# Performance work log

Measured on AMD Instinct MI355X. Metric: run time of the kernel, lower is better.

The kernel has to match this reference:

```python
import jax, jax.numpy as jnp
import numpy as np

N_NODES = 10000
N_EDGES = 640000
D = 128


def setup_inputs() -> dict:
    key = jax.random.key(0)
    k1, k2, k3, k4 = jax.random.split(key, 4)
    X = jax.random.normal(k1, (N_NODES, D), dtype=jnp.float32)
    Y = jax.random.normal(k2, (N_EDGES, D), dtype=jnp.float32)
    # nn.Linear(in, out, bias=False): weight shape (out, in), y = Y @ W.T
    W = jax.random.normal(k3, (D, D), dtype=jnp.float32) * (1.0 / np.sqrt(D))
    edge_index = jax.random.randint(k4, (N_EDGES, 2), 0, N_NODES, dtype=jnp.int64)
    return {"X": X, "Y": Y, "W": W, "edge_index": edge_index}


def reference(X, Y, W, edge_index):
    # Edge transform: (E, d_in) @ (d_in, d_out) -> (E, d_out)
    Y_prime = jnp.einsum('ei,oi->eo', Y, W)
    # Scatter-add transformed edge features to source nodes
    src = edge_index[:, 0]
    agg = jax.ops.segment_sum(Y_prime, src, num_segments=X.shape[0])  # (N, d_out)
    # Residual + activation
    X_prime = jax.nn.relu(X + agg)
    return (X_prime, Y_prime)
```

## Files before the change

### kernel.cpp

```cpp
#include <hip/hip_runtime.h>

#define N_NODES 10000
#define N_EDGES 640000
#define DD 128

typedef __attribute__((ext_vector_type(8))) short short8;
typedef __attribute__((ext_vector_type(8))) float f32x8;
typedef __attribute__((ext_vector_type(4))) float f32x4;
typedef __attribute__((ext_vector_type(2))) float f32x2;

__device__ __forceinline__ unsigned pack_bf2(float lo, float hi) {
  return __builtin_amdgcn_perm(__float_as_uint(hi), __float_as_uint(lo), 0x07060302u);
}

__device__ __forceinline__ void stage_w(const float* __restrict__ W,
                                        short8* lwr) {
  const int tid = threadIdx.x;
#pragma unroll
  for (int t = 0; t < 8; ++t) {
    int s = t * 256 + tid;
    f32x8 v = *(const f32x8*)(W + (size_t)s * 8);
    short8 av;
    unsigned* au = (unsigned*)&av;
    au[0] = pack_bf2(v[0], v[1]);
    au[1] = pack_bf2(v[2], v[3]);
    au[2] = pack_bf2(v[4], v[5]);
    au[3] = pack_bf2(v[6], v[7]);
    int j = s >> 4;
    int c = s & 15;
    lwr[(j << 4) | (c ^ (j & 7))] = av;
  }
  __syncthreads();
}

__global__ __launch_bounds__(256) void k_hist(const int* __restrict__ EI,
                                              int* __restrict__ count) {
  const int e = blockIdx.x * 256 + threadIdx.x;
  atomicAdd(&count[EI[2 * e]], 1);
}

__global__ __launch_bounds__(1024) void k_scan(const int* __restrict__ count,
                                               int* __restrict__ rowptr,
                                               int* __restrict__ cursor) {
  __shared__ int part[1024];
  const int tid = threadIdx.x;
  const int base = tid * 10;
  int local[10];
  int s = 0;
#pragma unroll
  for (int i = 0; i < 10; ++i) {
    const int idx = base + i;
    const int v = (idx < N_NODES) ? count[idx] : 0;
    local[i] = s;
    s += v;
  }
  part[tid] = s;
  __syncthreads();
  for (int off = 1; off < 1024; off <<= 1) {
    int v = 0;
    if (tid >= off) v = part[tid - off];
    __syncthreads();
    if (tid >= off) part[tid] += v;
    __syncthreads();
  }
  const int excl = (tid > 0) ? part[tid - 1] : 0;
#pragma unroll
  for (int i = 0; i < 10; ++i) {
    const int idx = base + i;
    if (idx < N_NODES) {
      const int r = excl + local[i];
      rowptr[idx] = r;
      cursor[idx] = r;
    }
  }
  if (tid == 1023) rowptr[N_NODES] = part[1023];
}

__global__ __launch_bounds__(256) void k_fill(const int* __restrict__ EI,
                                              int* __restrict__ cursor,
                                              int* __restrict__ col) {
  const int e = blockIdx.x * 256 + threadIdx.x;
  const int s = EI[2 * e];
  const int pos = atomicAdd(&cursor[s], 1);
  col[pos] = e;
}

__global__ __launch_bounds__(256, 2) void k_gemm_big(
    const float* __restrict__ Y,
    const float* __restrict__ W,
    float* __restrict__ Yp) {
  __shared__ short8 lwr[2048];
  stage_w(W, lwr);
  const int wid  = threadIdx.x >> 6;
  const int lane = threadIdx.x & 63;
  const int l15  = lane & 15;
  const int lg   = lane >> 4;
  const int koff = lg * 8;

#pragma unroll 1
  for (int ch = 0; ch < 2; ++ch) {
    const int ebase = (blockIdx.x * 2 + ch) * 128 + wid * 32;

    short8 a[2][4];
#pragma unroll
    for (int mt = 0; mt < 2; ++mt) {
      const float* yr = Y + (size_t)(ebase + mt * 16 + l15) * DD;
#pragma unroll
      for (int kk = 0; kk < 4; ++kk) {
        f32x8 v = *(const f32x8*)(yr + kk * 32 + koff);
        short8 av;
        unsigned* au = (unsigned*)&av;
        au[0] = pack_bf2(v[0], v[1]);
        au[1] = pack_bf2(v[2], v[3]);
        au[2] = pack_bf2(v[4], v[5]);
        au[3] = pack_bf2(v[6], v[7]);
        a[mt][kk] = av;
      }
    }

    f32x4 acc[2][8];
#pragma unroll
    for (int mt = 0; mt < 2; ++mt)
#pragma unroll
      for (int nt = 0; nt < 8; ++nt)
        acc[mt][nt] = (f32x4){0.f, 0.f, 0.f, 0.f};

#pragma unroll
    for (int nt = 0; nt < 8; ++nt) {
      const int j = nt * 16 + l15;
#pragma unroll
      for (int kk = 0; kk < 4; ++kk) {
        const int kc = kk * 4 + lg;
        short8 b = lwr[(j << 4) | (kc ^ (j & 7))];
        acc[0][nt] = __builtin_amdgcn_mfma_f32_16x16x32_bf16(a[0][kk], b, acc[0][nt], 0, 0, 0);
        acc[1][nt] = __builtin_amdgcn_mfma_f32_16x16x32_bf16(a[1][kk], b, acc[1][nt], 0, 0, 0);
      }
    }

    const int r0 = lg * 4;
#pragma unroll
    for (int mt = 0; mt < 2; ++mt) {
#pragma unroll
      for (int reg = 0; reg < 4; ++reg) {
        float* orow = Yp + (size_t)(ebase + mt * 16 + r0 + reg) * DD + l15;
#pragma unroll
        for (int nt = 0; nt < 8; ++nt)
          orow[nt * 16] = acc[mt][nt][reg];
      }
    }
  }
}

__global__ __launch_bounds__(256) void k_gather(
    const float* __restrict__ Yp,
    const int* __restrict__ rowptr,
    const int* __restrict__ col,
    const float* __restrict__ X,
    float* __restrict__ Xp) {
  const int node = blockIdx.x * 4 + (threadIdx.x >> 6);
  const int lane = threadIdx.x & 63;
  const size_t co = 2 * lane;
  const int b  = rowptr[node];
  const int en = rowptr[node + 1];

  f32x2 acc = *(const f32x2*)(X + (size_t)node * DD + co);
  int i = b;
  for (; i + 4 <= en; i += 4) {
    const int e0 = col[i], e1 = col[i + 1], e2 = col[i + 2], e3 = col[i + 3];
    f32x2 v0 = *(const f32x2*)(Yp + (size_t)e0 * DD + co);
    f32x2 v1 = *(const f32x2*)(Yp + (size_t)e1 * DD + co);
    f32x2 v2 = *(const f32x2*)(Yp + (size_t)e2 * DD + co);
    f32x2 v3 = *(const f32x2*)(Yp + (size_t)e3 * DD + co);
    acc += v0; acc += v1; acc += v2; acc += v3;
  }
  for (; i < en; ++i) {
    const int e0 = col[i];
    acc += *(const f32x2*)(Yp + (size_t)e0 * DD + co);
  }
  f32x2 r;
  r[0] = acc[0] > 0.f ? acc[0] : 0.f;
  r[1] = acc[1] > 0.f ? acc[1] : 0.f;
  *(f32x2*)(Xp + (size_t)node * DD + co) = r;
}

extern "C" void kernel_launch(void* const* d_in, const int* in_sizes, int n_in,
                              void* d_out, int out_size, void* d_ws, size_t ws_size,
                              hipStream_t stream) {
  const float* X  = (const float*)d_in[0];
  const float* Y  = (const float*)d_in[1];
  const float* W  = (const float*)d_in[2];
  const int*   EI = (const int*)d_in[3];

  float* Xp = (float*)d_out;
  float* Yp = Xp + (size_t)N_NODES * DD;

  int* w      = (int*)d_ws;
  int* count  = w;
  int* rowptr = w + 10000;
  int* cursor = w + 20001;
  int* col    = w + 30001;

  hipMemsetAsync(count, 0, N_NODES * sizeof(int), stream);
  k_hist<<<N_EDGES / 256, 256, 0, stream>>>(EI, count);
  k_scan<<<1, 1024, 0, stream>>>(count, rowptr, cursor);
  k_fill<<<N_EDGES / 256, 256, 0, stream>>>(EI, cursor, col);
  k_gemm_big<<<2500, 256, 0, stream>>>(Y, W, Yp);
  k_gather<<<2500, 256, 0, stream>>>(Yp, rowptr, col, X, Xp);
}
```

Baseline: 316.0 us.

## Use nontemporal Y loads, raise GEMM occupancy, unroll gather by 8, kernel memset

Several small tweaks at once. Y is read with nontemporal loads so it streams past the caches, and the GEMM launch bound moves from 2 to 4 blocks per CU. The gather loop unrolls to 8 edges to keep more loads in flight, and hipMemsetAsync is replaced by a small zeroing kernel. The tighter launch bound may force register spills in the GEMM, since each wave holds 16 accumulator vectors plus 8 A fragments.

```diff
diff --git a/kernel.cpp b/kernel.cpp
--- a/kernel.cpp
+++ b/kernel.cpp
@@ -33,6 +33,11 @@
   __syncthreads();
 }
 
+__global__ __launch_bounds__(256) void k_zero(int* __restrict__ count) {
+  const int i = blockIdx.x * 256 + threadIdx.x;
+  if (i < N_NODES) count[i] = 0;
+}
+
 __global__ __launch_bounds__(256) void k_hist(const int* __restrict__ EI,
                                               int* __restrict__ count) {
   const int e = blockIdx.x * 256 + threadIdx.x;
@@ -85,7 +90,7 @@
   col[pos] = e;
 }
 
-__global__ __launch_bounds__(256, 2) void k_gemm_big(
+__global__ __launch_bounds__(256, 4) void k_gemm_big(
     const float* __restrict__ Y,
     const float* __restrict__ W,
     float* __restrict__ Yp) {
@@ -107,13 +112,15 @@
       const float* yr = Y + (size_t)(ebase + mt * 16 + l15) * DD;
 #pragma unroll
       for (int kk = 0; kk < 4; ++kk) {
-        f32x8 v = *(const f32x8*)(yr + kk * 32 + koff);
+        const f32x4* p = (const f32x4*)(yr + kk * 32 + koff);
+        f32x4 v0 = __builtin_nontemporal_load(p);
+        f32x4 v1 = __builtin_nontemporal_load(p + 1);
         short8 av;
         unsigned* au = (unsigned*)&av;
-        au[0] = pack_bf2(v[0], v[1]);
-        au[1] = pack_bf2(v[2], v[3]);
-        au[2] = pack_bf2(v[4], v[5]);
-        au[3] = pack_bf2(v[6], v[7]);
+        au[0] = pack_bf2(v0[0], v0[1]);
+        au[1] = pack_bf2(v0[2], v0[3]);
+        au[2] = pack_bf2(v1[0], v1[1]);
+        au[3] = pack_bf2(v1[2], v1[3]);
         a[mt][kk] = av;
       }
     }
@@ -165,17 +172,20 @@
 
   f32x2 acc = *(const f32x2*)(X + (size_t)node * DD + co);
   int i = b;
-  for (; i + 4 <= en; i += 4) {
-    const int e0 = col[i], e1 = col[i + 1], e2 = col[i + 2], e3 = col[i + 3];
-    f32x2 v0 = *(const f32x2*)(Yp + (size_t)e0 * DD + co);
-    f32x2 v1 = *(const f32x2*)(Yp + (size_t)e1 * DD + co);
-    f32x2 v2 = *(const f32x2*)(Yp + (size_t)e2 * DD + co);
-    f32x2 v3 = *(const f32x2*)(Yp + (size_t)e3 * DD + co);
+  for (; i + 8 <= en; i += 8) {
+    f32x2 v0 = *(const f32x2*)(Yp + (size_t)col[i]     * DD + co);
+    f32x2 v1 = *(const f32x2*)(Yp + (size_t)col[i + 1] * DD + co);
+    f32x2 v2 = *(const f32x2*)(Yp + (size_t)col[i + 2] * DD + co);
+    f32x2 v3 = *(const f32x2*)(Yp + (size_t)col[i + 3] * DD + co);
+    f32x2 v4 = *(const f32x2*)(Yp + (size_t)col[i + 4] * DD + co);
+    f32x2 v5 = *(const f32x2*)(Yp + (size_t)col[i + 5] * DD + co);
+    f32x2 v6 = *(const f32x2*)(Yp + (size_t)col[i + 6] * DD + co);
+    f32x2 v7 = *(const f32x2*)(Yp + (size_t)col[i + 7] * DD + co);
     acc += v0; acc += v1; acc += v2; acc += v3;
+    acc += v4; acc += v5; acc += v6; acc += v7;
   }
   for (; i < en; ++i) {
-    const int e0 = col[i];
-    acc += *(const f32x2*)(Yp + (size_t)e0 * DD + co);
+    acc += *(const f32x2*)(Yp + (size_t)col[i] * DD + co);
   }
   f32x2 r;
   r[0] = acc[0] > 0.f ? acc[0] : 0.f;
@@ -200,7 +210,7 @@
   int* cursor = w + 20001;
   int* col    = w + 30001;
 
-  hipMemsetAsync(count, 0, N_NODES * sizeof(int), stream);
+  k_zero<<<(N_NODES + 255) / 256, 256, 0, stream>>>(count);
   k_hist<<<N_EDGES / 256, 256, 0, stream>>>(EI, count);
   k_scan<<<1, 1024, 0, stream>>>(count, rowptr, cursor);
   k_fill<<<N_EDGES / 256, 256, 0, stream>>>(EI, cursor, col);
```

Result: slower. 463.1 us (+46.5%).
